# Performance work log

Hardware: AMD Instinct MI355X
Metric: run time of the kernel (lower is better)

Reference implementation:

```python
import jax, jax.numpy as jnp
import numpy as np

UNITARY_SIZE = 128  # 2**7, gate acts on 7 qubits
N_QUBITS = 23
GATE_IDCS = [[0,1,2,3,4,5,6],[7,8,9,10,11,12,13],[3,5,7,9,11,13,15],[16,17,18,19,20,21,22]]


def setup_inputs() -> dict:
    key = jax.random.key(0)
    k1, k2 = jax.random.split(key)
    state = jax.random.normal(k1, (2, 2 ** N_QUBITS), dtype=jnp.float32)
    U = jax.random.normal(k2, (len(GATE_IDCS), 2, UNITARY_SIZE, UNITARY_SIZE), dtype=jnp.float32)
    return {"state": state, "U": U}


def _apply_gate(state, Ur, Ui, idcs, n):
    # permutation exactly as in run_circuit: targeted qubits to the front,
    # leading real/imag channel (dim 0) kept in place
    perm = [0] + [q + 1 for q in idcs + [q for q in range(n) if q not in idcs]]
    inv_perm = np.argsort(np.array(perm)).tolist()
    s = state.reshape((2,) + (2,) * n)
    s = jnp.transpose(s, perm)
    s = s.reshape(2, -1, UNITARY_SIZE)  # (channel, M, 128); matmul contracts last dim
    sr, si = s[0], s[1]
    # Karatsuba 3-matmul complex multiply, as in the NKI kernel
    Wr = jnp.einsum('ka,ma->mk', Ur, sr)
    Wi = jnp.einsum('ka,ma->mk', Ui, si)
    SASB = jnp.einsum('ka,ma->mk', Ur + Ui, sr + si)
    real = Wr - Wi
    imag = SASB - Wr - Wi
    # Faithful to the kernel: it stores the imag result into channel 0 and the
    # real result into channel 1 (swapped relative to the input convention).
    s = jnp.stack([imag, real], axis=0)
    s = s.reshape((2,) + (2,) * n)
    s = jnp.transpose(s, inv_perm)
    return s.reshape(2, -1)


def reference(state, U):
    for g, idcs in enumerate(GATE_IDCS):
        state = _apply_gate(state, U[g, 0], U[g, 1], idcs, N_QUBITS)
    return state
```

## Files before the change

kernel.cpp:

```cpp
#include <hip/hip_runtime.h>


typedef __attribute__((ext_vector_type(8))) short bf16x8;
typedef __attribute__((ext_vector_type(4))) short bf16x4;
typedef __attribute__((ext_vector_type(4))) float f32x4;

static constexpr int NSTATE = 1 << 23;

__device__ inline void tsplit(float x, unsigned short& h, unsigned short& l) {
    unsigned int u = __float_as_uint(x);
    h = (unsigned short)(u >> 16);
    float hf = __uint_as_float(u & 0xFFFF0000u);
    l = (unsigned short)(__float_as_uint(x - hf) >> 16);
}

__device__ inline void rsplit(float x, unsigned short& h, unsigned short& l) {
    unsigned int u = __float_as_uint(x);
    unsigned int r = (u + 0x7FFFu + ((u >> 16) & 1u)) >> 16;
    h = (unsigned short)r;
    float hf = __uint_as_float(r << 16);
    unsigned int u2 = __float_as_uint(x - hf);
    l = (unsigned short)((u2 + 0x7FFFu + ((u2 >> 16) & 1u)) >> 16);
}

__device__ inline float wElem(const float* __restrict__ Ug, int kp, int ap) {
    const int co = kp >> 7, ci = ap >> 7;
    const float v = Ug[((co == ci) ? 16384 : 0) + (kp & 127) * 128 + (ap & 127)];
    return (co & ci) ? -v : v;
}

__device__ inline int fragOff(int i, int t) {
    const int frag = (i >> 4) * 8 + (t >> 5);
    const int slot = (i & 15) + 16 * ((t >> 3) & 3);
    return frag * 512 + slot * 8 + (t & 7);
}

__device__ inline int slotSwz(int frag, int slot) {
    return slot ^ ((slot >> 3) & 6) ^ (frag & 7);
}

__device__ inline int sOff(int b, int kk) {
    const int frag = (b >> 4) * 8 + (kk >> 5);
    const int slot = (b & 15) + 16 * ((kk >> 3) & 3);
    return frag * 512 + slotSwz(frag, slot) * 8 + (kk & 7);
}

__global__ __launch_bounds__(256)
void prep_all(const float* __restrict__ U,
              unsigned short* __restrict__ WAh, unsigned short* __restrict__ WAl,
              unsigned short* __restrict__ WBh, unsigned short* __restrict__ WBl) {
    __shared__ float Arow[256];
    const int t = threadIdx.x;
    if (blockIdx.x < 256) {
        const int i = blockIdx.x;
        Arow[t] = wElem(U + 2 * 32768, i, t);
        __syncthreads();
        float r = 0.f;
        #pragma unroll 8
        for (int k = 0; k < 256; ++k)
            r = fmaf(Arow[k], wElem(U + 32768, k, t), r);
        __syncthreads();
        Arow[t] = r;
        __syncthreads();
        float s = 0.f;
        #pragma unroll 8
        for (int k = 0; k < 256; ++k)
            s = fmaf(Arow[k], wElem(U, k, t), s);
        unsigned short h, l;
        rsplit(s, h, l);
        const int off = fragOff(i, t);
        WAh[off] = h; WAl[off] = l;
    } else {
        const int i = blockIdx.x - 256;
        unsigned short h, l;
        rsplit(wElem(U + 3 * 32768, i, t), h, l);
        const int off = fragOff(i, t);
        WBh[off] = h; WBl[off] = l;
    }
}

__global__ __launch_bounds__(1024, 4)
void fused4(const float* __restrict__ src, float* __restrict__ dst,
            const unsigned short* __restrict__ WAh, const unsigned short* __restrict__ WAl,
            const unsigned short* __restrict__ WBh, const unsigned short* __restrict__ WBl)
{
    __shared__ unsigned short Sh[32768];
    __shared__ unsigned short Sl[32768];

    const int t    = threadIdx.x;
    const int lane = t & 63;
    const int w    = t >> 6;
    const int col  = lane & 15, quad = lane >> 4;
    const int mg   = w >> 3;
    const int ng   = w & 7;
    const int r0   = t >> 5;
    const int kkl  = (t & 31) * 4;

    float4 pf[8];

    #pragma unroll
    for (int hh = 0; hh < 2; ++hh) {
        const size_t hbase = (size_t)(blockIdx.x * 2 + hh) * 16384;

        {
            float4 v[8];
            if (hh == 0) {
                #pragma unroll
                for (int i = 0; i < 8; ++i) {
                    const int ch = i >> 2;
                    const int b  = (i & 3) * 32 + r0;
                    v[i] = *(const float4*)(src + (size_t)ch * NSTATE + hbase + (size_t)b * 128 + kkl);
                }
            } else {
                #pragma unroll
                for (int i = 0; i < 8; ++i) v[i] = pf[i];
            }
            #pragma unroll
            for (int i = 0; i < 8; ++i) {
                const int ch = i >> 2;
                const int b  = (i & 3) * 32 + r0;
                const int kk = ch * 128 + kkl;
                unsigned short h0, h1, h2, h3, l0, l1, l2s, l3;
                tsplit(v[i].x, h0, l0); tsplit(v[i].y, h1, l1);
                tsplit(v[i].z, h2, l2s); tsplit(v[i].w, h3, l3);
                const int off = sOff(b, kk);
                bf16x4 hv = { (short)h0, (short)h1, (short)h2, (short)h3 };
                bf16x4 lv = { (short)l0, (short)l1, (short)l2s, (short)l3 };
                *(bf16x4*)&Sh[off] = hv;
                *(bf16x4*)&Sl[off] = lv;
            }
        }
        __syncthreads();

        f32x4 acc[4][2];
        #pragma unroll
        for (int mi = 0; mi < 4; ++mi)
            #pragma unroll
            for (int l2 = 0; l2 < 2; ++l2) acc[mi][l2] = (f32x4)0.f;

        #pragma unroll 2
        for (int ks = 0; ks < 8; ++ks) {
            bf16x8 ah[4], al[4];
            #pragma unroll
            for (int mi = 0; mi < 4; ++mi) {
                const int fr = (mg * 4 + mi) * 8 + ks;
                const int fo = fr * 512 + slotSwz(fr, lane) * 8;
                ah[mi] = *(const bf16x8*)&Sh[fo];
                al[mi] = *(const bf16x8*)&Sl[fo];
            }
            bf16x8 bh[2], bl[2];
            #pragma unroll
            for (int l2 = 0; l2 < 2; ++l2) {
                const int fo = ((ng * 2 + l2) * 8 + ks) * 512 + lane * 8;
                bh[l2] = *(const bf16x8*)(WAh + fo);
                bl[l2] = *(const bf16x8*)(WAl + fo);
            }
            #pragma unroll
            for (int l2 = 0; l2 < 2; ++l2)
                #pragma unroll
                for (int mi = 0; mi < 4; ++mi) {
                    acc[mi][l2] = __builtin_amdgcn_mfma_f32_16x16x32_bf16(ah[mi], bh[l2], acc[mi][l2], 0, 0, 0);
                    acc[mi][l2] = __builtin_amdgcn_mfma_f32_16x16x32_bf16(al[mi], bh[l2], acc[mi][l2], 0, 0, 0);
                    acc[mi][l2] = __builtin_amdgcn_mfma_f32_16x16x32_bf16(ah[mi], bl[l2], acc[mi][l2], 0, 0, 0);
                }
        }
        __syncthreads();

        #pragma unroll
        for (int mi = 0; mi < 4; ++mi) {
            const int mt  = mg * 4 + mi;
            const int oct = (mt * 2 + (quad >> 1)) & 3;
            #pragma unroll
            for (int l2 = 0; l2 < 2; ++l2) {
                const int nt    = ng * 2 + l2;
                const int frag2 = (nt & 7) * 8 + (nt >> 3) * 4 + (mt >> 1);
                const int slot2 = col + 16 * oct;
                const int soff  = frag2 * 512 + slotSwz(frag2, slot2) * 8 + (quad & 1) * 4;
                unsigned short hhs[4], lls[4];
                #pragma unroll
                for (int r = 0; r < 4; ++r) tsplit(acc[mi][l2][r], hhs[r], lls[r]);
                bf16x4 hv = { (short)hhs[0], (short)hhs[1], (short)hhs[2], (short)hhs[3] };
                bf16x4 lv = { (short)lls[0], (short)lls[1], (short)lls[2], (short)lls[3] };
                *(bf16x4*)&Sh[soff] = hv;
                *(bf16x4*)&Sl[soff] = lv;
            }
        }
        __syncthreads();

        if (hh == 0) {
            const size_t hb1 = (size_t)(blockIdx.x * 2 + 1) * 16384;
            #pragma unroll
            for (int i = 0; i < 8; ++i) {
                const int ch = i >> 2;
                const int b  = (i & 3) * 32 + r0;
                pf[i] = *(const float4*)(src + (size_t)ch * NSTATE + hb1 + (size_t)b * 128 + kkl);
            }
        }

        f32x4 acc2[4][2];
        #pragma unroll
        for (int mi = 0; mi < 4; ++mi)
            #pragma unroll
            for (int nj = 0; nj < 2; ++nj) acc2[mi][nj] = (f32x4)0.f;

        #pragma unroll 2
        for (int ks2 = 0; ks2 < 8; ++ks2) {
            bf16x8 a2h[4], a2l[4];
            #pragma unroll
            for (int mi = 0; mi < 4; ++mi) {
                const int fr = (mg * 4 + mi) * 8 + ks2;
                const int fo = fr * 512 + slotSwz(fr, lane) * 8;
                a2h[mi] = *(const bf16x8*)&Sh[fo];
                a2l[mi] = *(const bf16x8*)&Sl[fo];
            }
            bf16x8 bh2[2], bl2[2];
            #pragma unroll
            for (int nj = 0; nj < 2; ++nj) {
                const int fo = ((ng * 2 + nj) * 8 + ks2) * 512 + lane * 8;
                bh2[nj] = *(const bf16x8*)(WBh + fo);
                bl2[nj] = *(const bf16x8*)(WBl + fo);
            }
            #pragma unroll
            for (int nj = 0; nj < 2; ++nj)
                #pragma unroll
                for (int mi = 0; mi < 4; ++mi) {
                    acc2[mi][nj] = __builtin_amdgcn_mfma_f32_16x16x32_bf16(a2h[mi], bh2[nj], acc2[mi][nj], 0, 0, 0);
                    acc2[mi][nj] = __builtin_amdgcn_mfma_f32_16x16x32_bf16(a2l[mi], bh2[nj], acc2[mi][nj], 0, 0, 0);
                    acc2[mi][nj] = __builtin_amdgcn_mfma_f32_16x16x32_bf16(a2h[mi], bl2[nj], acc2[mi][nj], 0, 0, 0);
                }
        }

        if (hh == 0) __syncthreads();

        #pragma unroll
        for (int nj = 0; nj < 2; ++nj) {
            const int kp2  = (ng * 2 + nj) * 16 + col;
            const int chpp = kp2 >> 7, kb = kp2 & 127;
            float* o = dst + (size_t)chpp * NSTATE + hbase + (size_t)kb * 128;
            #pragma unroll
            for (int mi = 0; mi < 4; ++mi) {
                const int ka = (mg * 4 + mi) * 16 + quad * 4;
                *(float4*)(o + ka) = *(float4*)&acc2[mi][nj];
            }
        }
    }
}

extern "C" void kernel_launch(void* const* d_in, const int* in_sizes, int n_in,
                              void* d_out, int out_size, void* d_ws, size_t ws_size,
                              hipStream_t stream) {
    const float* state = (const float*)d_in[0];
    const float* U     = (const float*)d_in[1];
    float* out = (float*)d_out;

    unsigned short* WAh = (unsigned short*)d_ws;
    unsigned short* WAl = WAh + 65536;
    unsigned short* WBh = WAh + 2 * 65536;
    unsigned short* WBl = WAh + 3 * 65536;

    prep_all<<<512, 256, 0, stream>>>(U, WAh, WAl, WBh, WBl);
    fused4  <<<256, 1024, 0, stream>>>(state, out, WAh, WAl, WBh, WBl);
}
```

Baseline: 183.7 us.

## Split fused kernel to one tile per block and prefetch weight fragments

Each block now handles one 16384-element tile instead of two, so the grid doubles to 512 blocks. The manual cross-tile register prefetch of the next tile's input is dropped. The main loops are fully unrolled with the high weight fragment double-buffered one k-step ahead, and the MFMAs are reordered into three grouped passes to break accumulator dependency chains. This trades the in-block load/compute overlap for more blocks per CU and better latency hiding across blocks.

Result: faster. 170.2 us (-7.4%).

```diff
diff --git a/kernel.cpp b/kernel.cpp
--- a/kernel.cpp
+++ b/kernel.cpp
@@ -80,7 +80,7 @@
 }
 
 __global__ __launch_bounds__(1024, 4)
-void fused4(const float* __restrict__ src, float* __restrict__ dst,
+void fused5(const float* __restrict__ src, float* __restrict__ dst,
             const unsigned short* __restrict__ WAh, const unsigned short* __restrict__ WAl,
             const unsigned short* __restrict__ WBh, const unsigned short* __restrict__ WBl)
 {
@@ -93,53 +93,51 @@
     const int col  = lane & 15, quad = lane >> 4;
     const int mg   = w >> 3;
     const int ng   = w & 7;
-    const int r0   = t >> 5;
-    const int kkl  = (t & 31) * 4;
-
-    float4 pf[8];
-
-    #pragma unroll
-    for (int hh = 0; hh < 2; ++hh) {
-        const size_t hbase = (size_t)(blockIdx.x * 2 + hh) * 16384;
-
-        {
-            float4 v[8];
-            if (hh == 0) {
-                #pragma unroll
-                for (int i = 0; i < 8; ++i) {
-                    const int ch = i >> 2;
-                    const int b  = (i & 3) * 32 + r0;
-                    v[i] = *(const float4*)(src + (size_t)ch * NSTATE + hbase + (size_t)b * 128 + kkl);
-                }
-            } else {
-                #pragma unroll
-                for (int i = 0; i < 8; ++i) v[i] = pf[i];
-            }
-            #pragma unroll
-            for (int i = 0; i < 8; ++i) {
-                const int ch = i >> 2;
-                const int b  = (i & 3) * 32 + r0;
-                const int kk = ch * 128 + kkl;
-                unsigned short h0, h1, h2, h3, l0, l1, l2s, l3;
-                tsplit(v[i].x, h0, l0); tsplit(v[i].y, h1, l1);
-                tsplit(v[i].z, h2, l2s); tsplit(v[i].w, h3, l3);
-                const int off = sOff(b, kk);
-                bf16x4 hv = { (short)h0, (short)h1, (short)h2, (short)h3 };
-                bf16x4 lv = { (short)l0, (short)l1, (short)l2s, (short)l3 };
-                *(bf16x4*)&Sh[off] = hv;
-                *(bf16x4*)&Sl[off] = lv;
-            }
-        }
-        __syncthreads();
-
-        f32x4 acc[4][2];
-        #pragma unroll
-        for (int mi = 0; mi < 4; ++mi)
-            #pragma unroll
-            for (int l2 = 0; l2 < 2; ++l2) acc[mi][l2] = (f32x4)0.f;
-
-        #pragma unroll 2
+    const size_t hbase = (size_t)blockIdx.x * 16384;
+
+    {
+        const int r0  = t >> 5;
+        const int kkl = (t & 31) * 4;
+        float4 v[8];
+        #pragma unroll
+        for (int i = 0; i < 8; ++i) {
+            const int ch = i >> 2;
+            const int b  = (i & 3) * 32 + r0;
+            v[i] = *(const float4*)(src + (size_t)ch * NSTATE + hbase + (size_t)b * 128 + kkl);
+        }
+        #pragma unroll
+        for (int i = 0; i < 8; ++i) {
+            const int ch = i >> 2;
+            const int b  = (i & 3) * 32 + r0;
+            const int kk = ch * 128 + kkl;
+            unsigned short h0, h1, h2, h3, l0, l1, l2s, l3;
+            tsplit(v[i].x, h0, l0); tsplit(v[i].y, h1, l1);
+            tsplit(v[i].z, h2, l2s); tsplit(v[i].w, h3, l3);
+            const int off = sOff(b, kk);
+            bf16x4 hv = { (short)h0, (short)h1, (short)h2, (short)h3 };
+            bf16x4 lv = { (short)l0, (short)l1, (short)l2s, (short)l3 };
+            *(bf16x4*)&Sh[off] = hv;
+            *(bf16x4*)&Sl[off] = lv;
+        }
+    }
+    __syncthreads();
+
+    f32x4 acc[4][2];
+    #pragma unroll
+    for (int mi = 0; mi < 4; ++mi)
+        #pragma unroll
+        for (int l2 = 0; l2 < 2; ++l2) acc[mi][l2] = (f32x4)0.f;
+
+    {
+        bf16x8 bh[2][2];
+        #pragma unroll
+        for (int l2 = 0; l2 < 2; ++l2) {
+            const int fo = ((ng * 2 + l2) * 8 + 0) * 512 + lane * 8;
+            bh[0][l2] = *(const bf16x8*)(WAh + fo);
+        }
+        #pragma unroll
         for (int ks = 0; ks < 8; ++ks) {
+            const int cur = ks & 1, nxt = cur ^ 1;
             bf16x8 ah[4], al[4];
             #pragma unroll
             for (int mi = 0; mi < 4; ++mi) {
@@ -148,63 +146,75 @@
                 ah[mi] = *(const bf16x8*)&Sh[fo];
                 al[mi] = *(const bf16x8*)&Sl[fo];
             }
-            bf16x8 bh[2], bl[2];
+            bf16x8 bl[2];
             #pragma unroll
             for (int l2 = 0; l2 < 2; ++l2) {
                 const int fo = ((ng * 2 + l2) * 8 + ks) * 512 + lane * 8;
-                bh[l2] = *(const bf16x8*)(WAh + fo);
                 bl[l2] = *(const bf16x8*)(WAl + fo);
             }
+            if (ks < 7) {
+                #pragma unroll
+                for (int l2 = 0; l2 < 2; ++l2) {
+                    const int fo = ((ng * 2 + l2) * 8 + (ks + 1)) * 512 + lane * 8;
+                    bh[nxt][l2] = *(const bf16x8*)(WAh + fo);
+                }
+            }
             #pragma unroll
             for (int l2 = 0; l2 < 2; ++l2)
                 #pragma unroll
-                for (int mi = 0; mi < 4; ++mi) {
-                    acc[mi][l2] = __builtin_amdgcn_mfma_f32_16x16x32_bf16(ah[mi], bh[l2], acc[mi][l2], 0, 0, 0);
-                    acc[mi][l2] = __builtin_amdgcn_mfma_f32_16x16x32_bf16(al[mi], bh[l2], acc[mi][l2], 0, 0, 0);
+                for (int mi = 0; mi < 4; ++mi)
+                    acc[mi][l2] = __builtin_amdgcn_mfma_f32_16x16x32_bf16(ah[mi], bh[cur][l2], acc[mi][l2], 0, 0, 0);
+            #pragma unroll
+            for (int l2 = 0; l2 < 2; ++l2)
+                #pragma unroll
+                for (int mi = 0; mi < 4; ++mi)
+                    acc[mi][l2] = __builtin_amdgcn_mfma_f32_16x16x32_bf16(al[mi], bh[cur][l2], acc[mi][l2], 0, 0, 0);
+            #pragma unroll
+            for (int l2 = 0; l2 < 2; ++l2)
+                #pragma unroll
+                for (int mi = 0; mi < 4; ++mi)
                     acc[mi][l2] = __builtin_amdgcn_mfma_f32_16x16x32_bf16(ah[mi], bl[l2], acc[mi][l2], 0, 0, 0);
-                }
-        }
-        __syncthreads();
-
-        #pragma unroll
-        for (int mi = 0; mi < 4; ++mi) {
-            const int mt  = mg * 4 + mi;
-            const int oct = (mt * 2 + (quad >> 1)) & 3;
-            #pragma unroll
-            for (int l2 = 0; l2 < 2; ++l2) {
-                const int nt    = ng * 2 + l2;
-                const int frag2 = (nt & 7) * 8 + (nt >> 3) * 4 + (mt >> 1);
-                const int slot2 = col + 16 * oct;
-                const int soff  = frag2 * 512 + slotSwz(frag2, slot2) * 8 + (quad & 1) * 4;
-                unsigned short hhs[4], lls[4];
-                #pragma unroll
-                for (int r = 0; r < 4; ++r) tsplit(acc[mi][l2][r], hhs[r], lls[r]);
-                bf16x4 hv = { (short)hhs[0], (short)hhs[1], (short)hhs[2], (short)hhs[3] };
-                bf16x4 lv = { (short)lls[0], (short)lls[1], (short)lls[2], (short)lls[3] };
-                *(bf16x4*)&Sh[soff] = hv;
-                *(bf16x4*)&Sl[soff] = lv;
-            }
-        }
-        __syncthreads();
-
-        if (hh == 0) {
-            const size_t hb1 = (size_t)(blockIdx.x * 2 + 1) * 16384;
-            #pragma unroll
-            for (int i = 0; i < 8; ++i) {
-                const int ch = i >> 2;
-                const int b  = (i & 3) * 32 + r0;
-                pf[i] = *(const float4*)(src + (size_t)ch * NSTATE + hb1 + (size_t)b * 128 + kkl);
-            }
-        }
-
-        f32x4 acc2[4][2];
-        #pragma unroll
-        for (int mi = 0; mi < 4; ++mi)
-            #pragma unroll
-            for (int nj = 0; nj < 2; ++nj) acc2[mi][nj] = (f32x4)0.f;
-
-        #pragma unroll 2
+        }
+    }
+    __syncthreads();
+
+    #pragma unroll
+    for (int mi = 0; mi < 4; ++mi) {
+        const int mt  = mg * 4 + mi;
+        const int oct = (mt * 2 + (quad >> 1)) & 3;
+        #pragma unroll
+        for (int l2 = 0; l2 < 2; ++l2) {
+            const int nt    = ng * 2 + l2;
+            const int frag2 = (nt & 7) * 8 + (nt >> 3) * 4 + (mt >> 1);
+            const int slot2 = col + 16 * oct;
+            const int soff  = frag2 * 512 + slotSwz(frag2, slot2) * 8 + (quad & 1) * 4;
+            unsigned short hhs[4], lls[4];
+            #pragma unroll
+            for (int r = 0; r < 4; ++r) tsplit(acc[mi][l2][r], hhs[r], lls[r]);
+            bf16x4 hv = { (short)hhs[0], (short)hhs[1], (short)hhs[2], (short)hhs[3] };
+            bf16x4 lv = { (short)lls[0], (short)lls[1], (short)lls[2], (short)lls[3] };
+            *(bf16x4*)&Sh[soff] = hv;
+            *(bf16x4*)&Sl[soff] = lv;
+        }
+    }
+    __syncthreads();
+
+    f32x4 acc2[4][2];
+    #pragma unroll
+    for (int mi = 0; mi < 4; ++mi)
+        #pragma unroll
+        for (int nj = 0; nj < 2; ++nj) acc2[mi][nj] = (f32x4)0.f;
+
+    {
+        bf16x8 bh2[2][2];
+        #pragma unroll
+        for (int nj = 0; nj < 2; ++nj) {
+            const int fo = ((ng * 2 + nj) * 8 + 0) * 512 + lane * 8;
+            bh2[0][nj] = *(const bf16x8*)(WBh + fo);
+        }
+        #pragma unroll
         for (int ks2 = 0; ks2 < 8; ++ks2) {
+            const int cur = ks2 & 1, nxt = cur ^ 1;
             bf16x8 a2h[4], a2l[4];
             #pragma unroll
             for (int mi = 0; mi < 4; ++mi) {
@@ -213,35 +223,46 @@
                 a2h[mi] = *(const bf16x8*)&Sh[fo];
                 a2l[mi] = *(const bf16x8*)&Sl[fo];
             }
-            bf16x8 bh2[2], bl2[2];
+            bf16x8 bl2[2];
             #pragma unroll
             for (int nj = 0; nj < 2; ++nj) {
                 const int fo = ((ng * 2 + nj) * 8 + ks2) * 512 + lane * 8;
-                bh2[nj] = *(const bf16x8*)(WBh + fo);
                 bl2[nj] = *(const bf16x8*)(WBl + fo);
             }
+            if (ks2 < 7) {
+                #pragma unroll
+                for (int nj = 0; nj < 2; ++nj) {
+                    const int fo = ((ng * 2 + nj) * 8 + (ks2 + 1)) * 512 + lane * 8;
+                    bh2[nxt][nj] = *(const bf16x8*)(WBh + fo);
+                }
+            }
             #pragma unroll
             for (int nj = 0; nj < 2; ++nj)
                 #pragma unroll
-                for (int mi = 0; mi < 4; ++mi) {
-                    acc2[mi][nj] = __builtin_amdgcn_mfma_f32_16x16x32_bf16(a2h[mi], bh2[nj], acc2[mi][nj], 0, 0, 0);
-                    acc2[mi][nj] = __builtin_amdgcn_mfma_f32_16x16x32_bf16(a2l[mi], bh2[nj], acc2[mi][nj], 0, 0, 0);
+                for (int mi = 0; mi < 4; ++mi)
+                    acc2[mi][nj] = __builtin_amdgcn_mfma_f32_16x16x32_bf16(a2h[mi], bh2[cur][nj], acc2[mi][nj], 0, 0, 0);
+            #pragma unroll
+            for (int nj = 0; nj < 2; ++nj)
+                #pragma unroll
+                for (int mi = 0; mi < 4; ++mi)
+                    acc2[mi][nj] = __builtin_amdgcn_mfma_f32_16x16x32_bf16(a2l[mi], bh2[cur][nj], acc2[mi][nj], 0, 0, 0);
+            #pragma unroll
+            for (int nj = 0; nj < 2; ++nj)
+                #pragma unroll
+                for (int mi = 0; mi < 4; ++mi)
                     acc2[mi][nj] = __builtin_amdgcn_mfma_f32_16x16x32_bf16(a2h[mi], bl2[nj], acc2[mi][nj], 0, 0, 0);
-                }
-        }
-
-        if (hh == 0) __syncthreads();
-
-        #pragma unroll
-        for (int nj = 0; nj < 2; ++nj) {
-            const int kp2  = (ng * 2 + nj) * 16 + col;
-            const int chpp = kp2 >> 7, kb = kp2 & 127;
-            float* o = dst + (size_t)chpp * NSTATE + hbase + (size_t)kb * 128;
-            #pragma unroll
-            for (int mi = 0; mi < 4; ++mi) {
-                const int ka = (mg * 4 + mi) * 16 + quad * 4;
-                *(float4*)(o + ka) = *(float4*)&acc2[mi][nj];
-            }
+        }
+    }
+
+    #pragma unroll
+    for (int nj = 0; nj < 2; ++nj) {
+        const int kp2  = (ng * 2 + nj) * 16 + col;
+        const int chpp = kp2 >> 7, kb = kp2 & 127;
+        float* o = dst + (size_t)chpp * NSTATE + hbase + (size_t)kb * 128;
+        #pragma unroll
+        for (int mi = 0; mi < 4; ++mi) {
+            const int ka = (mg * 4 + mi) * 16 + quad * 4;
+            *(float4*)(o + ka) = *(float4*)&acc2[mi][nj];
         }
     }
 }
@@ -259,5 +280,5 @@
     unsigned short* WBl = WAh + 3 * 65536;
 
     prep_all<<<512, 256, 0, stream>>>(U, WAh, WAl, WBh, WBl);
-    fused4  <<<256, 1024, 0, stream>>>(state, out, WAh, WAl, WBh, WBl);
-}
+    fused5 <<<512, 1024, 0, stream>>>(state, out, WAh, WAl, WBh, WBl);
+}
```

## Load state tiles via global_load_lds DMA and split to bf16 at fragment read

Applied to the files above, without the earlier changes.

Replaces the register-staged global loads and the bf16 hi/lo split-at-store with direct global-to-LDS DMA of raw fp32 rows into an XOR-swizzled buffer. The split into hi/lo happens when each MFMA fragment is read. Each block now handles one 16384-element slab instead of two, so the grid doubles to 512 and the manual cross-half prefetch is dropped. The per-wave tile changes to 2x4 MFMA tiles, and the MFMA issue order is regrouped into three passes. The aim is to cut VGPR staging and conversion work on the load path and to overlap the second channel's load with the first half of the k-loop, at the cost of losing the explicit prefetch pipeline.

After: 167.5 us. -8.8%, faster.

```diff
diff --git a/kernel.cpp b/kernel.cpp
--- a/kernel.cpp
+++ b/kernel.cpp
@@ -12,6 +12,15 @@
     h = (unsigned short)(u >> 16);
     float hf = __uint_as_float(u & 0xFFFF0000u);
     l = (unsigned short)(__float_as_uint(x - hf) >> 16);
+}
+
+__device__ inline void split8(const float* xv, bf16x8& hv, bf16x8& lv) {
+    #pragma unroll
+    for (int i = 0; i < 8; ++i) {
+        unsigned short h, l;
+        tsplit(xv[i], h, l);
+        hv[i] = (short)h; lv[i] = (short)l;
+    }
 }
 
 __device__ inline void rsplit(float x, unsigned short& h, unsigned short& l) {
@@ -39,10 +48,11 @@
     return slot ^ ((slot >> 3) & 6) ^ (frag & 7);
 }
 
-__device__ inline int sOff(int b, int kk) {
-    const int frag = (b >> 4) * 8 + (kk >> 5);
-    const int slot = (b & 15) + 16 * ((kk >> 3) & 3);
-    return frag * 512 + slotSwz(frag, slot) * 8 + (kk & 7);
+__device__ inline void dma16(const float* gp, float* lp) {
+    __builtin_amdgcn_global_load_lds(
+        (const __attribute__((address_space(1))) unsigned int*)gp,
+        (__attribute__((address_space(3))) unsigned int*)lp,
+        16, 0, 0);
 }
 
 __global__ __launch_bounds__(256)
@@ -80,168 +90,157 @@
 }
 
 __global__ __launch_bounds__(1024, 4)
-void fused4(const float* __restrict__ src, float* __restrict__ dst,
+void fused6(const float* __restrict__ src, float* __restrict__ dst,
             const unsigned short* __restrict__ WAh, const unsigned short* __restrict__ WAl,
             const unsigned short* __restrict__ WBh, const unsigned short* __restrict__ WBl)
 {
-    __shared__ unsigned short Sh[32768];
-    __shared__ unsigned short Sl[32768];
+    __shared__ unsigned short S[65536];
+    float* Sf            = (float*)S;
+    unsigned short* Mh   = S;
+    unsigned short* Ml   = S + 32768;
 
     const int t    = threadIdx.x;
     const int lane = t & 63;
     const int w    = t >> 6;
     const int col  = lane & 15, quad = lane >> 4;
-    const int mg   = w >> 3;
-    const int ng   = w & 7;
-    const int r0   = t >> 5;
-    const int kkl  = (t & 31) * 4;
-
-    float4 pf[8];
-
-    #pragma unroll
-    for (int hh = 0; hh < 2; ++hh) {
-        const size_t hbase = (size_t)(blockIdx.x * 2 + hh) * 16384;
-
-        {
-            float4 v[8];
-            if (hh == 0) {
-                #pragma unroll
-                for (int i = 0; i < 8; ++i) {
-                    const int ch = i >> 2;
-                    const int b  = (i & 3) * 32 + r0;
-                    v[i] = *(const float4*)(src + (size_t)ch * NSTATE + hbase + (size_t)b * 128 + kkl);
-                }
-            } else {
-                #pragma unroll
-                for (int i = 0; i < 8; ++i) v[i] = pf[i];
-            }
-            #pragma unroll
-            for (int i = 0; i < 8; ++i) {
-                const int ch = i >> 2;
-                const int b  = (i & 3) * 32 + r0;
-                const int kk = ch * 128 + kkl;
-                unsigned short h0, h1, h2, h3, l0, l1, l2s, l3;
-                tsplit(v[i].x, h0, l0); tsplit(v[i].y, h1, l1);
-                tsplit(v[i].z, h2, l2s); tsplit(v[i].w, h3, l3);
-                const int off = sOff(b, kk);
-                bf16x4 hv = { (short)h0, (short)h1, (short)h2, (short)h3 };
-                bf16x4 lv = { (short)l0, (short)l1, (short)l2s, (short)l3 };
-                *(bf16x4*)&Sh[off] = hv;
-                *(bf16x4*)&Sl[off] = lv;
-            }
-        }
-        __syncthreads();
-
-        f32x4 acc[4][2];
-        #pragma unroll
-        for (int mi = 0; mi < 4; ++mi)
-            #pragma unroll
-            for (int l2 = 0; l2 < 2; ++l2) acc[mi][l2] = (f32x4)0.f;
-
-        #pragma unroll 2
-        for (int ks = 0; ks < 8; ++ks) {
-            bf16x8 ah[4], al[4];
-            #pragma unroll
-            for (int mi = 0; mi < 4; ++mi) {
-                const int fr = (mg * 4 + mi) * 8 + ks;
-                const int fo = fr * 512 + slotSwz(fr, lane) * 8;
-                ah[mi] = *(const bf16x8*)&Sh[fo];
-                al[mi] = *(const bf16x8*)&Sl[fo];
-            }
-            bf16x8 bh[2], bl[2];
-            #pragma unroll
-            for (int l2 = 0; l2 < 2; ++l2) {
-                const int fo = ((ng * 2 + l2) * 8 + ks) * 512 + lane * 8;
-                bh[l2] = *(const bf16x8*)(WAh + fo);
-                bl[l2] = *(const bf16x8*)(WAl + fo);
-            }
-            #pragma unroll
-            for (int l2 = 0; l2 < 2; ++l2)
-                #pragma unroll
-                for (int mi = 0; mi < 4; ++mi) {
-                    acc[mi][l2] = __builtin_amdgcn_mfma_f32_16x16x32_bf16(ah[mi], bh[l2], acc[mi][l2], 0, 0, 0);
-                    acc[mi][l2] = __builtin_amdgcn_mfma_f32_16x16x32_bf16(al[mi], bh[l2], acc[mi][l2], 0, 0, 0);
-                    acc[mi][l2] = __builtin_amdgcn_mfma_f32_16x16x32_bf16(ah[mi], bl[l2], acc[mi][l2], 0, 0, 0);
-                }
-        }
-        __syncthreads();
-
-        #pragma unroll
-        for (int mi = 0; mi < 4; ++mi) {
-            const int mt  = mg * 4 + mi;
-            const int oct = (mt * 2 + (quad >> 1)) & 3;
-            #pragma unroll
-            for (int l2 = 0; l2 < 2; ++l2) {
-                const int nt    = ng * 2 + l2;
-                const int frag2 = (nt & 7) * 8 + (nt >> 3) * 4 + (mt >> 1);
-                const int slot2 = col + 16 * oct;
-                const int soff  = frag2 * 512 + slotSwz(frag2, slot2) * 8 + (quad & 1) * 4;
-                unsigned short hhs[4], lls[4];
-                #pragma unroll
-                for (int r = 0; r < 4; ++r) tsplit(acc[mi][l2][r], hhs[r], lls[r]);
-                bf16x4 hv = { (short)hhs[0], (short)hhs[1], (short)hhs[2], (short)hhs[3] };
-                bf16x4 lv = { (short)lls[0], (short)lls[1], (short)lls[2], (short)lls[3] };
-                *(bf16x4*)&Sh[soff] = hv;
-                *(bf16x4*)&Sl[soff] = lv;
-            }
-        }
-        __syncthreads();
-
-        if (hh == 0) {
-            const size_t hb1 = (size_t)(blockIdx.x * 2 + 1) * 16384;
-            #pragma unroll
-            for (int i = 0; i < 8; ++i) {
-                const int ch = i >> 2;
-                const int b  = (i & 3) * 32 + r0;
-                pf[i] = *(const float4*)(src + (size_t)ch * NSTATE + hb1 + (size_t)b * 128 + kkl);
-            }
-        }
-
-        f32x4 acc2[4][2];
-        #pragma unroll
-        for (int mi = 0; mi < 4; ++mi)
-            #pragma unroll
-            for (int nj = 0; nj < 2; ++nj) acc2[mi][nj] = (f32x4)0.f;
-
-        #pragma unroll 2
-        for (int ks2 = 0; ks2 < 8; ++ks2) {
-            bf16x8 a2h[4], a2l[4];
-            #pragma unroll
-            for (int mi = 0; mi < 4; ++mi) {
-                const int fr = (mg * 4 + mi) * 8 + ks2;
-                const int fo = fr * 512 + slotSwz(fr, lane) * 8;
-                a2h[mi] = *(const bf16x8*)&Sh[fo];
-                a2l[mi] = *(const bf16x8*)&Sl[fo];
-            }
-            bf16x8 bh2[2], bl2[2];
-            #pragma unroll
-            for (int nj = 0; nj < 2; ++nj) {
-                const int fo = ((ng * 2 + nj) * 8 + ks2) * 512 + lane * 8;
-                bh2[nj] = *(const bf16x8*)(WBh + fo);
-                bl2[nj] = *(const bf16x8*)(WBl + fo);
-            }
-            #pragma unroll
-            for (int nj = 0; nj < 2; ++nj)
-                #pragma unroll
-                for (int mi = 0; mi < 4; ++mi) {
-                    acc2[mi][nj] = __builtin_amdgcn_mfma_f32_16x16x32_bf16(a2h[mi], bh2[nj], acc2[mi][nj], 0, 0, 0);
-                    acc2[mi][nj] = __builtin_amdgcn_mfma_f32_16x16x32_bf16(a2l[mi], bh2[nj], acc2[mi][nj], 0, 0, 0);
-                    acc2[mi][nj] = __builtin_amdgcn_mfma_f32_16x16x32_bf16(a2h[mi], bl2[nj], acc2[mi][nj], 0, 0, 0);
-                }
-        }
-
-        if (hh == 0) __syncthreads();
-
-        #pragma unroll
-        for (int nj = 0; nj < 2; ++nj) {
-            const int kp2  = (ng * 2 + nj) * 16 + col;
-            const int chpp = kp2 >> 7, kb = kp2 & 127;
-            float* o = dst + (size_t)chpp * NSTATE + hbase + (size_t)kb * 128;
-            #pragma unroll
-            for (int mi = 0; mi < 4; ++mi) {
-                const int ka = (mg * 4 + mi) * 16 + quad * 4;
-                *(float4*)(o + ka) = *(float4*)&acc2[mi][nj];
-            }
+    const int mg   = w & 3;
+    const int ng   = w >> 2;
+    const size_t hbase = (size_t)blockIdx.x * 16384;
+
+    #pragma unroll
+    for (int j = 0; j < 4; ++j) {
+        const int r0 = w * 8 + (j & 3) * 2;
+        const int r  = r0 + (lane >> 5);
+        const int cb = ((lane & 31) << 4) ^ ((r & 7) << 4);
+        dma16(src + hbase + (size_t)r * 128 + (cb >> 2), Sf + r0 * 128);
+    }
+    __syncthreads();
+    #pragma unroll
+    for (int j = 4; j < 8; ++j) {
+        const int r0 = 128 + w * 8 + (j & 3) * 2;
+        const int r  = r0 + (lane >> 5);
+        const int cb = ((lane & 31) << 4) ^ ((r & 7) << 4);
+        dma16(src + (size_t)NSTATE + hbase + (size_t)(r & 127) * 128 + (cb >> 2),
+              Sf + r0 * 128);
+    }
+
+    f32x4 acc[2][4];
+    #pragma unroll
+    for (int mi = 0; mi < 2; ++mi)
+        #pragma unroll
+        for (int nj = 0; nj < 4; ++nj) acc[mi][nj] = (f32x4)0.f;
+
+    #pragma unroll
+    for (int ks = 0; ks < 8; ++ks) {
+        if (ks == 4) __syncthreads();
+        const int ch  = ks >> 2;
+        const int cb0 = (ks & 3) * 128 + quad * 32;
+        bf16x8 ah[2], al[2];
+        #pragma unroll
+        for (int mi = 0; mi < 2; ++mi) {
+            const int r   = ch * 128 + (mg * 2 + mi) * 16 + col;
+            const int swz = (r & 7) << 4;
+            const char* rowp = (const char*)Sf + r * 512;
+            float xv[8];
+            *(float4*)&xv[0] = *(const float4*)(rowp + (cb0 ^ swz));
+            *(float4*)&xv[4] = *(const float4*)(rowp + ((cb0 + 16) ^ swz));
+            split8(xv, ah[mi], al[mi]);
+        }
+        bf16x8 bh[4], bl[4];
+        #pragma unroll
+        for (int nj = 0; nj < 4; ++nj) {
+            const int fo = ((ng * 4 + nj) * 8 + ks) * 512 + lane * 8;
+            bh[nj] = *(const bf16x8*)(WAh + fo);
+            bl[nj] = *(const bf16x8*)(WAl + fo);
+        }
+        #pragma unroll
+        for (int nj = 0; nj < 4; ++nj)
+            #pragma unroll
+            for (int mi = 0; mi < 2; ++mi)
+                acc[mi][nj] = __builtin_amdgcn_mfma_f32_16x16x32_bf16(ah[mi], bh[nj], acc[mi][nj], 0, 0, 0);
+        #pragma unroll
+        for (int nj = 0; nj < 4; ++nj)
+            #pragma unroll
+            for (int mi = 0; mi < 2; ++mi)
+                acc[mi][nj] = __builtin_amdgcn_mfma_f32_16x16x32_bf16(al[mi], bh[nj], acc[mi][nj], 0, 0, 0);
+        #pragma unroll
+        for (int nj = 0; nj < 4; ++nj)
+            #pragma unroll
+            for (int mi = 0; mi < 2; ++mi)
+                acc[mi][nj] = __builtin_amdgcn_mfma_f32_16x16x32_bf16(ah[mi], bl[nj], acc[mi][nj], 0, 0, 0);
+    }
+    __syncthreads();
+
+    #pragma unroll
+    for (int mi = 0; mi < 2; ++mi) {
+        const int mt  = mg * 2 + mi;
+        const int oct = (mt * 2 + (quad >> 1)) & 3;
+        #pragma unroll
+        for (int nj = 0; nj < 4; ++nj) {
+            const int nt    = ng * 4 + nj;
+            const int frag2 = (nt & 7) * 8 + (nt >> 3) * 4 + (mt >> 1);
+            const int slot2 = col + 16 * oct;
+            const int soff  = frag2 * 512 + slotSwz(frag2, slot2) * 8 + (quad & 1) * 4;
+            unsigned short hhs[4], lls[4];
+            #pragma unroll
+            for (int r = 0; r < 4; ++r) tsplit(acc[mi][nj][r], hhs[r], lls[r]);
+            bf16x4 hv = { (short)hhs[0], (short)hhs[1], (short)hhs[2], (short)hhs[3] };
+            bf16x4 lv = { (short)lls[0], (short)lls[1], (short)lls[2], (short)lls[3] };
+            *(bf16x4*)&Mh[soff] = hv;
+            *(bf16x4*)&Ml[soff] = lv;
+        }
+    }
+    __syncthreads();
+
+    f32x4 acc2[2][4];
+    #pragma unroll
+    for (int mi = 0; mi < 2; ++mi)
+        #pragma unroll
+        for (int nj = 0; nj < 4; ++nj) acc2[mi][nj] = (f32x4)0.f;
+
+    #pragma unroll
+    for (int ks2 = 0; ks2 < 8; ++ks2) {
+        bf16x8 a2h[2], a2l[2];
+        #pragma unroll
+        for (int mi = 0; mi < 2; ++mi) {
+            const int fr = (mg * 2 + mi) * 8 + ks2;
+            const int fo = fr * 512 + slotSwz(fr, lane) * 8;
+            a2h[mi] = *(const bf16x8*)&Mh[fo];
+            a2l[mi] = *(const bf16x8*)&Ml[fo];
+        }
+        bf16x8 bh2[4], bl2[4];
+        #pragma unroll
+        for (int nj = 0; nj < 4; ++nj) {
+            const int fo = ((ng * 4 + nj) * 8 + ks2) * 512 + lane * 8;
+            bh2[nj] = *(const bf16x8*)(WBh + fo);
+            bl2[nj] = *(const bf16x8*)(WBl + fo);
+        }
+        #pragma unroll
+        for (int nj = 0; nj < 4; ++nj)
+            #pragma unroll
+            for (int mi = 0; mi < 2; ++mi)
+                acc2[mi][nj] = __builtin_amdgcn_mfma_f32_16x16x32_bf16(a2h[mi], bh2[nj], acc2[mi][nj], 0, 0, 0);
+        #pragma unroll
+        for (int nj = 0; nj < 4; ++nj)
+            #pragma unroll
+            for (int mi = 0; mi < 2; ++mi)
+                acc2[mi][nj] = __builtin_amdgcn_mfma_f32_16x16x32_bf16(a2l[mi], bh2[nj], acc2[mi][nj], 0, 0, 0);
+        #pragma unroll
+        for (int nj = 0; nj < 4; ++nj)
+            #pragma unroll
+            for (int mi = 0; mi < 2; ++mi)
+                acc2[mi][nj] = __builtin_amdgcn_mfma_f32_16x16x32_bf16(a2h[mi], bl2[nj], acc2[mi][nj], 0, 0, 0);
+    }
+
+    #pragma unroll
+    for (int nj = 0; nj < 4; ++nj) {
+        const int kp2  = (ng * 4 + nj) * 16 + col;
+        const int chpp = kp2 >> 7, kb = kp2 & 127;
+        float* o = dst + (size_t)chpp * NSTATE + hbase + (size_t)kb * 128;
+        #pragma unroll
+        for (int mi = 0; mi < 2; ++mi) {
+            const int ka = (mg * 2 + mi) * 16 + quad * 4;
+            *(float4*)(o + ka) = *(float4*)&acc2[mi][nj];
         }
     }
 }
@@ -259,5 +258,5 @@
     unsigned short* WBl = WAh + 3 * 65536;
 
     prep_all<<<512, 256, 0, stream>>>(U, WAh, WAl, WBh, WBl);
-    fused4  <<<256, 1024, 0, stream>>>(state, out, WAh, WAl, WBh, WBl);
-}
+    fused6 <<<512, 1024, 0, stream>>>(state, out, WAh, WAl, WBh, WBl);
+}
```
